# Kernel optimization log

Measured on AMD Instinct MI355X. Metric: run time of the kernel, lower is better.

## Reference

```python
import jax, jax.numpy as jnp
import numpy as np

N, C, B = 65536, 512, 4
H, P = 8, 256           # num_heads, patch_size
D = C // H              # head_dim = 64


def setup_inputs() -> dict:
    key = jax.random.key(0)
    k0, k1, k2 = jax.random.split(key, 3)
    x = jax.random.normal(k0, (N, C), dtype=jnp.float32)
    # sorted batch ids, equal-sized scenes (each divisible by patch_size)
    batch = (jnp.arange(N) // (N // B)).astype(jnp.int32)
    w_qkv = jax.random.normal(k1, (C, 3 * C), dtype=jnp.float32) * (C ** -0.5)
    b_qkv = jnp.zeros((3 * C,), dtype=jnp.float32)
    w_proj = jax.random.normal(k2, (C, C), dtype=jnp.float32) * (C ** -0.5)
    b_proj = jnp.zeros((C,), dtype=jnp.float32)
    return {"x": x, "batch": batch, "w_qkv": w_qkv, "b_qkv": b_qkv,
            "w_proj": w_proj, "b_proj": b_proj}


def reference(x, batch, w_qkv, b_qkv, w_proj, b_proj):
    # batch is sorted with per-scene counts divisible by P, so the original
    # per-batch mask/pad loop is exactly a global reshape into patches.
    n = x.shape[0]
    scale = D ** -0.5
    qkv = (x @ w_qkv + b_qkv).reshape(n, 3, H, D)
    q, k, v = qkv[:, 0], qkv[:, 1], qkv[:, 2]          # (N, H, D)
    q = q.reshape(-1, P, H, D)                          # (nP, P, H, D)
    k = k.reshape(-1, P, H, D)
    v = v.reshape(-1, P, H, D)
    attn = jnp.einsum('pihd,pjhd->phij', q, k) * scale  # (nP, H, P, P)
    attn = jax.nn.softmax(attn, axis=-1)
    out = jnp.einsum('phij,pjhd->pihd', attn, v)        # (nP, P, H, D)
    out = out.reshape(n, C)
    return out @ w_proj + b_proj
```

## Files before the change

kernel.cpp:

```cpp
#include <hip/hip_runtime.h>
#include <hip/hip_bf16.h>
#include <cstdint>

typedef __attribute__((ext_vector_type(8))) short bf16x8;
typedef __attribute__((ext_vector_type(4))) float f32x4;
typedef unsigned short u16;
typedef unsigned int u32;

#define MFMA16(a, b, c) __builtin_amdgcn_mfma_f32_16x16x32_bf16(a, b, c, 0, 0, 0)

__device__ __forceinline__ u16 f2bf(float f) {
  u32 u = __builtin_bit_cast(u32, f);
  u32 r = (u + 0x7fffu + ((u >> 16) & 1u)) >> 16;
  return (u16)r;
}

__device__ __forceinline__ void gload_lds16(const u16* g, u16* l) {
  __builtin_amdgcn_global_load_lds(
      (const __attribute__((address_space(1))) u32*)(const void*)g,
      (__attribute__((address_space(3))) u32*)(void*)l, 16, 0, 0);
}


__global__ __launch_bounds__(256) void cvt_x_kernel(const float* __restrict__ in,
                                                    u16* __restrict__ out, int n4) {
  const int stride = gridDim.x * blockDim.x;
  for (int i = blockIdx.x * blockDim.x + threadIdx.x; i < n4; i += stride) {
    float4 v = ((const float4*)in)[i];
    ushort4 o;
    o.x = f2bf(v.x); o.y = f2bf(v.y); o.z = f2bf(v.z); o.w = f2bf(v.w);
    ((ushort4*)out)[i] = o;
  }
}

__global__ __launch_bounds__(256) void transpose_kernel(const float* __restrict__ in,
                                                        u16* __restrict__ out,
                                                        int rows, int cols) {
  int idx = blockIdx.x * 256 + threadIdx.x;
  if (idx < rows * cols) {
    int c = idx / rows, r = idx - c * rows;
    out[idx] = f2bf(in[(size_t)r * cols + c]);
  }
}


template <bool OUT_BF16, int NTN>
__global__ __launch_bounds__(512, 2) void gemm8(const u16* __restrict__ A,
                                                const u16* __restrict__ Bt,
                                                const float* __restrict__ bias,
                                                void* __restrict__ Cout, int Ncols) {
  constexpr int K = 512;
  const int nwg = gridDim.x;
  const int q8 = nwg >> 3;
  const int L = (blockIdx.x & 7) * q8 + (blockIdx.x >> 3);
  const int tm = L / NTN, tn = L % NTN;

  const int t = threadIdx.x, lane = t & 63, w = t >> 6;
  const int wr = w >> 2, wc = w & 3;
  const int fr = lane & 15, fq = lane >> 4;

  __shared__ __align__(16) u16 lds[2][2][2][8192];

  const u16* Ab = A + (size_t)tm * 256 * K;
  const u16* Bb = Bt + (size_t)tn * 256 * K;

  int srow[2], scol[2];
#pragma unroll
  for (int i = 0; i < 2; ++i) {
    const int cidx = t + i * 512;
    const int rr = cidx >> 7, cc = (cidx >> 6) & 1, r16 = (cidx >> 2) & 15, qq = cidx & 3;
    const int c8 = qq ^ ((r16 >> 3) << 1);
    srow[i] = rr * 16 + r16;
    scol[i] = cc * 32 + c8 * 8;
  }

  f32x4 acc[8][4] = {};
  bf16x8 areg[4][2];
  bf16x8 breg[4][2];

  const int swz = (fq * 16) ^ ((fr & 8) << 2);

#define STAGE(SB, SOP, SH, STK)                                                  \
  {                                                                              \
    const u16* gb_ = (SOP == 0) ? Ab : Bb;                                       \
    u16* lb_ = &lds[SB][SOP][SH][0];                                             \
    _Pragma("unroll") for (int i_ = 0; i_ < 2; ++i_) {                           \
      gload_lds16(gb_ + (size_t)(SH * 128 + srow[i_]) * K + (STK) * 64 + scol[i_],\
                  lb_ + (t + i_ * 512) * 8);                                     \
    }                                                                            \
  }

#define LDA(RB, MH)                                                              \
  {                                                                              \
    const char* ab_ = (const char*)&lds[RB][0][wr][0];                           \
    _Pragma("unroll") for (int m_ = 0; m_ < 4; ++m_)                             \
      _Pragma("unroll") for (int kk_ = 0; kk_ < 2; ++kk_)                        \
        areg[m_][kk_] = *(const bf16x8*)(ab_ + ((MH) * 4 + m_) * 2048 +          \
                                         kk_ * 1024 + fr * 64 + swz);            \
  }

#define LDB(RB, NH)                                                              \
  {                                                                              \
    const char* bb_ = (const char*)&lds[RB][1][wc >> 1][0];                      \
    _Pragma("unroll") for (int n_ = 0; n_ < 2; ++n_)                             \
      _Pragma("unroll") for (int kk_ = 0; kk_ < 2; ++kk_)                        \
        breg[(NH) * 2 + n_][kk_] = *(const bf16x8*)(bb_ +                        \
            ((wc & 1) * 4 + (NH) * 2 + n_) * 2048 + kk_ * 1024 + fr * 64 + swz); \
  }

#define MMA(MH, NH)                                                              \
  {                                                                              \
    __builtin_amdgcn_s_setprio(1);                                               \
    _Pragma("unroll") for (int m_ = 0; m_ < 4; ++m_)                             \
      _Pragma("unroll") for (int n_ = 0; n_ < 2; ++n_)                           \
        _Pragma("unroll") for (int kk_ = 0; kk_ < 2; ++kk_)                      \
          acc[(MH) * 4 + m_][(NH) * 2 + n_] =                                    \
              MFMA16(areg[m_][kk_], breg[(NH) * 2 + n_][kk_],                    \
                     acc[(MH) * 4 + m_][(NH) * 2 + n_]);                         \
    __builtin_amdgcn_s_setprio(0);                                               \
  }

#define BAR() __builtin_amdgcn_s_barrier()
#define WLGKM() asm volatile("s_waitcnt lgkmcnt(0)" ::: "memory")
#define WV4() asm volatile("s_waitcnt vmcnt(4)" ::: "memory")
#define WV0() asm volatile("s_waitcnt vmcnt(0)" ::: "memory")

  STAGE(0, 1, 0, 0) STAGE(0, 1, 1, 0) STAGE(0, 0, 0, 0) STAGE(0, 0, 1, 0)
  STAGE(1, 1, 0, 1) STAGE(1, 1, 1, 1)
  WV4();
  BAR();

#pragma unroll 1
  for (int s = 0; s < 3; ++s) {
    const int o1 = 2 * s + 1, e2 = 2 * s + 2, o3 = 2 * s + 3;
    LDA(0, 0) LDB(0, 0) STAGE(1, 0, 0, o1) BAR(); WLGKM(); MMA(0, 0) BAR();
    LDB(0, 1) STAGE(1, 0, 1, o1) BAR(); WLGKM(); MMA(0, 1) BAR();
    LDA(0, 1) STAGE(0, 1, 0, e2) BAR(); WLGKM(); MMA(1, 0) BAR();
    STAGE(0, 1, 1, e2) BAR(); MMA(1, 1) WV4(); BAR();
    LDA(1, 0) LDB(1, 0) STAGE(0, 0, 0, e2) BAR(); WLGKM(); MMA(0, 0) BAR();
    LDB(1, 1) STAGE(0, 0, 1, e2) BAR(); WLGKM(); MMA(0, 1) BAR();
    LDA(1, 1) STAGE(1, 1, 0, o3) BAR(); WLGKM(); MMA(1, 0) BAR();
    STAGE(1, 1, 1, o3) BAR(); MMA(1, 1) WV4(); BAR();
  }
  LDA(0, 0) LDB(0, 0) STAGE(1, 0, 0, 7) BAR(); WLGKM(); MMA(0, 0) BAR();
  LDB(0, 1) STAGE(1, 0, 1, 7) BAR(); WLGKM(); MMA(0, 1) BAR();
  LDA(0, 1) BAR(); WLGKM(); MMA(1, 0) BAR();
  BAR(); MMA(1, 1) WV0(); BAR();
  LDA(1, 0) LDB(1, 0) BAR(); WLGKM(); MMA(0, 0) BAR();
  LDB(1, 1) BAR(); WLGKM(); MMA(0, 1) BAR();
  LDA(1, 1) BAR(); WLGKM(); MMA(1, 0) BAR();
  MMA(1, 1)

#pragma unroll
  for (int nt = 0; nt < 4; ++nt) {
    const int col = tn * 256 + wc * 64 + nt * 16 + fr;
    const float bv = bias[col];
#pragma unroll
    for (int mt = 0; mt < 8; ++mt) {
#pragma unroll
      for (int r = 0; r < 4; ++r) {
        const int row = tm * 256 + wr * 128 + mt * 16 + fq * 4 + r;
        float v = acc[mt][nt][r] + bv;
        if (OUT_BF16)
          ((u16*)Cout)[(size_t)row * Ncols + col] = f2bf(v);
        else
          ((float*)Cout)[(size_t)row * Ncols + col] = v;
      }
    }
  }
#undef STAGE
#undef LDA
#undef LDB
#undef MMA
#undef BAR
#undef WLGKM
#undef WV4
#undef WV0
}


__global__ __launch_bounds__(512) void attn_kernel(const u16* __restrict__ qkv,
                                                   u16* __restrict__ out) {
  const int p = blockIdx.x, h = blockIdx.y;
  const int t = threadIdx.x, lane = t & 63, w = t >> 6;
  const int fr = lane & 15, fq = lane >> 4;

  __shared__ __align__(16) u16 Kls[256][72];
  __shared__ __align__(16) u16 Vt[64][264];
  __shared__ __align__(16) u16 Pls[8][32][72];

  const u16* base = qkv + (size_t)p * 256 * 1536 + h * 64;

#pragma unroll
  for (int it = 0; it < 4; ++it) {
    int chunk = it * 512 + t;
    int row = chunk >> 3, c8 = (chunk & 7) * 8;
    *(uint4*)&Kls[row][c8] = *(const uint4*)(base + (size_t)row * 1536 + 512 + c8);
  }
  {
    int token = t & 255, dh = (t >> 8) * 32;
    const u16* vs = base + (size_t)token * 1536 + 1024 + dh;
    uint4 b0 = *(const uint4*)(vs);
    uint4 b1 = *(const uint4*)(vs + 8);
    uint4 b2 = *(const uint4*)(vs + 16);
    uint4 b3 = *(const uint4*)(vs + 24);
    u16 tmp[32];
    *(uint4*)&tmp[0] = b0; *(uint4*)&tmp[8] = b1;
    *(uint4*)&tmp[16] = b2; *(uint4*)&tmp[24] = b3;
#pragma unroll
    for (int dd = 0; dd < 32; ++dd) Vt[dh + dd][token] = tmp[dd];
  }
  bf16x8 qf[2][2];
#pragma unroll
  for (int mt = 0; mt < 2; ++mt)
#pragma unroll
    for (int kk = 0; kk < 2; ++kk)
      qf[mt][kk] = *(const bf16x8*)(base + (size_t)(w * 32 + mt * 16 + fr) * 1536 + kk * 32 + fq * 8);
  __syncthreads();

  f32x4 Oc[2][4] = {};
  float mrow[2][4], lrow[2][4];
#pragma unroll
  for (int mt = 0; mt < 2; ++mt)
#pragma unroll
    for (int r = 0; r < 4; ++r) { mrow[mt][r] = -1e30f; lrow[mt][r] = 0.f; }

  for (int jb = 0; jb < 4; ++jb) {
    f32x4 S[2][4] = {};
#pragma unroll
    for (int kk = 0; kk < 2; ++kk) {
      bf16x8 kb[4];
#pragma unroll
      for (int jt = 0; jt < 4; ++jt)
        kb[jt] = *(const bf16x8*)&Kls[jb * 64 + jt * 16 + fr][kk * 32 + fq * 8];
#pragma unroll
      for (int mt = 0; mt < 2; ++mt)
#pragma unroll
        for (int jt = 0; jt < 4; ++jt)
          S[mt][jt] = MFMA16(qf[mt][kk], kb[jt], S[mt][jt]);
    }
#pragma unroll
    for (int mt = 0; mt < 2; ++mt) {
#pragma unroll
      for (int r = 0; r < 4; ++r) {
        float s0 = S[mt][0][r] * 0.125f, s1 = S[mt][1][r] * 0.125f;
        float s2 = S[mt][2][r] * 0.125f, s3 = S[mt][3][r] * 0.125f;
        float mx = fmaxf(fmaxf(s0, s1), fmaxf(s2, s3));
#pragma unroll
        for (int d = 1; d < 16; d <<= 1) mx = fmaxf(mx, __shfl_xor(mx, d, 64));
        float mnew = fmaxf(mrow[mt][r], mx);
        float alpha = __expf(mrow[mt][r] - mnew);
        mrow[mt][r] = mnew;
        float e0 = __expf(s0 - mnew), e1 = __expf(s1 - mnew);
        float e2 = __expf(s2 - mnew), e3 = __expf(s3 - mnew);
        S[mt][0][r] = e0; S[mt][1][r] = e1; S[mt][2][r] = e2; S[mt][3][r] = e3;
        float rs = e0 + e1 + e2 + e3;
#pragma unroll
        for (int d = 1; d < 16; d <<= 1) rs += __shfl_xor(rs, d, 64);
        lrow[mt][r] = lrow[mt][r] * alpha + rs;
#pragma unroll
        for (int dt = 0; dt < 4; ++dt) Oc[mt][dt][r] *= alpha;
      }
    }
#pragma unroll
    for (int mt = 0; mt < 2; ++mt)
#pragma unroll
      for (int jt = 0; jt < 4; ++jt)
#pragma unroll
        for (int r = 0; r < 4; ++r)
          Pls[w][mt * 16 + fq * 4 + r][jt * 16 + fr] = f2bf(S[mt][jt][r]);
    __syncthreads();
#pragma unroll
    for (int kk = 0; kk < 2; ++kk) {
      bf16x8 pa[2], vb[4];
#pragma unroll
      for (int mt = 0; mt < 2; ++mt)
        pa[mt] = *(const bf16x8*)&Pls[w][mt * 16 + fr][kk * 32 + fq * 8];
#pragma unroll
      for (int dt = 0; dt < 4; ++dt)
        vb[dt] = *(const bf16x8*)&Vt[dt * 16 + fr][jb * 64 + kk * 32 + fq * 8];
#pragma unroll
      for (int mt = 0; mt < 2; ++mt)
#pragma unroll
        for (int dt = 0; dt < 4; ++dt)
          Oc[mt][dt] = MFMA16(pa[mt], vb[dt], Oc[mt][dt]);
    }
  }
#pragma unroll
  for (int mt = 0; mt < 2; ++mt) {
#pragma unroll
    for (int r = 0; r < 4; ++r) {
      const float inv = 1.0f / lrow[mt][r];
      const int token = p * 256 + w * 32 + mt * 16 + fq * 4 + r;
#pragma unroll
      for (int dt = 0; dt < 4; ++dt)
        out[(size_t)token * 512 + h * 64 + dt * 16 + fr] = f2bf(Oc[mt][dt][r] * inv);
    }
  }
}


extern "C" void kernel_launch(void* const* d_in, const int* in_sizes, int n_in,
                              void* d_out, int out_size, void* d_ws, size_t ws_size,
                              hipStream_t stream) {
  const float* x      = (const float*)d_in[0];
  const float* w_qkv  = (const float*)d_in[2];
  const float* b_qkv  = (const float*)d_in[3];
  const float* w_proj = (const float*)d_in[4];
  const float* b_proj = (const float*)d_in[5];

  char* ws = (char*)d_ws;
  u16* xa     = (u16*)ws;
  u16* wqkvT  = (u16*)(ws + 67108864);
  u16* wprojT = (u16*)(ws + 68681728);
  u16* qkv    = (u16*)(ws + 69206016);
  u16* attn   = xa;

  cvt_x_kernel<<<2048, 256, 0, stream>>>(x, xa, 65536 * 512 / 4);
  transpose_kernel<<<(512 * 1536 + 255) / 256, 256, 0, stream>>>(w_qkv, wqkvT, 512, 1536);
  transpose_kernel<<<(512 * 512 + 255) / 256, 256, 0, stream>>>(w_proj, wprojT, 512, 512);

  gemm8<true, 6><<<1536, 512, 0, stream>>>(xa, wqkvT, b_qkv, qkv, 1536);
  attn_kernel<<<dim3(256, 8), 512, 0, stream>>>(qkv, attn);
  gemm8<false, 2><<<512, 512, 0, stream>>>(attn, wprojT, b_proj, d_out, 512);
}
```

Before: 590.7 us.

## Replace online softmax with full-row softmax held in registers in attention

After: 541.8 us. 8.3% less time.

```diff
diff --git a/kernel.cpp b/kernel.cpp
--- a/kernel.cpp
+++ b/kernel.cpp
@@ -179,8 +179,8 @@
 }
 
 
-__global__ __launch_bounds__(512) void attn_kernel(const u16* __restrict__ qkv,
-                                                   u16* __restrict__ out) {
+__global__ __launch_bounds__(512, 2) void attn_kernel(const u16* __restrict__ qkv,
+                                                      u16* __restrict__ out) {
   const int p = blockIdx.x, h = blockIdx.y;
   const int t = threadIdx.x, lane = t & 63, w = t >> 6;
   const int fr = lane & 15, fq = lane >> 4;
@@ -218,15 +218,9 @@
       qf[mt][kk] = *(const bf16x8*)(base + (size_t)(w * 32 + mt * 16 + fr) * 1536 + kk * 32 + fq * 8);
   __syncthreads();
 
-  f32x4 Oc[2][4] = {};
-  float mrow[2][4], lrow[2][4];
-#pragma unroll
-  for (int mt = 0; mt < 2; ++mt)
-#pragma unroll
-    for (int r = 0; r < 4; ++r) { mrow[mt][r] = -1e30f; lrow[mt][r] = 0.f; }
-
+  f32x4 S[2][16] = {};
+#pragma unroll
   for (int jb = 0; jb < 4; ++jb) {
-    f32x4 S[2][4] = {};
 #pragma unroll
     for (int kk = 0; kk < 2; ++kk) {
       bf16x8 kb[4];
@@ -237,39 +231,52 @@
       for (int mt = 0; mt < 2; ++mt)
 #pragma unroll
         for (int jt = 0; jt < 4; ++jt)
-          S[mt][jt] = MFMA16(qf[mt][kk], kb[jt], S[mt][jt]);
-    }
-#pragma unroll
-    for (int mt = 0; mt < 2; ++mt) {
-#pragma unroll
-      for (int r = 0; r < 4; ++r) {
-        float s0 = S[mt][0][r] * 0.125f, s1 = S[mt][1][r] * 0.125f;
-        float s2 = S[mt][2][r] * 0.125f, s3 = S[mt][3][r] * 0.125f;
-        float mx = fmaxf(fmaxf(s0, s1), fmaxf(s2, s3));
-#pragma unroll
-        for (int d = 1; d < 16; d <<= 1) mx = fmaxf(mx, __shfl_xor(mx, d, 64));
-        float mnew = fmaxf(mrow[mt][r], mx);
-        float alpha = __expf(mrow[mt][r] - mnew);
-        mrow[mt][r] = mnew;
-        float e0 = __expf(s0 - mnew), e1 = __expf(s1 - mnew);
-        float e2 = __expf(s2 - mnew), e3 = __expf(s3 - mnew);
-        S[mt][0][r] = e0; S[mt][1][r] = e1; S[mt][2][r] = e2; S[mt][3][r] = e3;
-        float rs = e0 + e1 + e2 + e3;
-#pragma unroll
-        for (int d = 1; d < 16; d <<= 1) rs += __shfl_xor(rs, d, 64);
-        lrow[mt][r] = lrow[mt][r] * alpha + rs;
-#pragma unroll
-        for (int dt = 0; dt < 4; ++dt) Oc[mt][dt][r] *= alpha;
+          S[mt][jb * 4 + jt] = MFMA16(qf[mt][kk], kb[jt], S[mt][jb * 4 + jt]);
+    }
+  }
+
+  float lrow[2][4];
+#pragma unroll
+  for (int mt = 0; mt < 2; ++mt) {
+#pragma unroll
+    for (int r = 0; r < 4; ++r) {
+      float v[16];
+#pragma unroll
+      for (int j = 0; j < 16; ++j) v[j] = S[mt][j][r] * 0.125f;
+      float m8[8];
+#pragma unroll
+      for (int j = 0; j < 8; ++j) m8[j] = fmaxf(v[2 * j], v[2 * j + 1]);
+      float m4a = fmaxf(m8[0], m8[1]), m4b = fmaxf(m8[2], m8[3]);
+      float m4c = fmaxf(m8[4], m8[5]), m4d = fmaxf(m8[6], m8[7]);
+      float mx = fmaxf(fmaxf(m4a, m4b), fmaxf(m4c, m4d));
+#pragma unroll
+      for (int d = 1; d < 16; d <<= 1) mx = fmaxf(mx, __shfl_xor(mx, d, 64));
+      float s8[8];
+#pragma unroll
+      for (int j = 0; j < 8; ++j) {
+        float e0 = __expf(v[2 * j] - mx), e1 = __expf(v[2 * j + 1] - mx);
+        S[mt][2 * j][r] = e0; S[mt][2 * j + 1][r] = e1;
+        s8[j] = e0 + e1;
       }
-    }
+      float s4a = s8[0] + s8[1], s4b = s8[2] + s8[3];
+      float s4c = s8[4] + s8[5], s4d = s8[6] + s8[7];
+      float sum = (s4a + s4b) + (s4c + s4d);
+#pragma unroll
+      for (int d = 1; d < 16; d <<= 1) sum += __shfl_xor(sum, d, 64);
+      lrow[mt][r] = sum;
+    }
+  }
+
+  f32x4 Oc[2][4] = {};
+#pragma unroll
+  for (int jb = 0; jb < 4; ++jb) {
 #pragma unroll
     for (int mt = 0; mt < 2; ++mt)
 #pragma unroll
       for (int jt = 0; jt < 4; ++jt)
 #pragma unroll
         for (int r = 0; r < 4; ++r)
-          Pls[w][mt * 16 + fq * 4 + r][jt * 16 + fr] = f2bf(S[mt][jt][r]);
-    __syncthreads();
+          Pls[w][mt * 16 + fq * 4 + r][jt * 16 + fr] = f2bf(S[mt][jb * 4 + jt][r]);
 #pragma unroll
     for (int kk = 0; kk < 2; ++kk) {
       bf16x8 pa[2], vb[4];
@@ -286,6 +293,7 @@
           Oc[mt][dt] = MFMA16(pa[mt], vb[dt], Oc[mt][dt]);
     }
   }
+
 #pragma unroll
   for (int mt = 0; mt < 2; ++mt) {
 #pragma unroll
```
